# Performance work log

Hardware: AMD Instinct MI355X
Metric: run time of the kernel (lower is better)

Reference implementation:

```python
import jax, jax.numpy as jnp
import numpy as np

N = 100000      # nodes
F_IN = 500      # num_features
H = 128         # num_hidden
C = 40          # num_classes
E = 3200000     # structural edges
K = 5           # knn neighbors


def setup_inputs() -> dict:
    key = jax.random.key(0)
    ks = jax.random.split(key, 9)
    x = jax.random.normal(ks[0], (N, F_IN), dtype=jnp.float32)
    edge_index = jax.random.randint(ks[1], (2, E), 0, N, dtype=jnp.int64)
    # knn graph: source i repeated K times, targets random (stand-in for cosine-KNN)
    src = jnp.repeat(jnp.arange(N, dtype=jnp.int64), K)
    dst = jax.random.randint(ks[2], (K * N,), 0, N, dtype=jnp.int64)
    edge_index_knn = jnp.stack([src, dst])
    s = lambda f: np.float32(1.0 / np.sqrt(f))
    W1 = jax.random.normal(ks[3], (F_IN, H), jnp.float32) * s(F_IN)
    b1 = jnp.zeros((H,), jnp.float32)
    W2 = jax.random.normal(ks[4], (2 * H, C), jnp.float32) * s(2 * H)
    b2 = jnp.zeros((C,), jnp.float32)
    Wlin = jax.random.normal(ks[5], (C, 2 * C), jnp.float32) * s(2 * C)  # torch Linear layout [out,in]
    blin = jnp.zeros((C,), jnp.float32)
    return {"x": x, "edge_index": edge_index, "edge_index_knn": edge_index_knn,
            "W1": W1, "b1": b1, "W2": W2, "b2": b2, "Wlin": Wlin, "blin": blin}


def gcn_conv(x, W, b, edge_index):
    # PyG GCNConv: add self-loops, symmetric normalization deg^-1/2 A deg^-1/2, x@W, scatter-add, +bias
    n = x.shape[0]
    loop = jnp.arange(n, dtype=edge_index.dtype)
    row = jnp.concatenate([edge_index[0], loop])  # sources (gathered)
    col = jnp.concatenate([edge_index[1], loop])  # targets (scattered)
    deg = jax.ops.segment_sum(jnp.ones_like(col, x.dtype), col, num_segments=n)
    dinv = jnp.where(deg > 0, jax.lax.rsqrt(jnp.maximum(deg, 1e-12)), 0.0).astype(x.dtype)
    norm = dinv[row] * dinv[col]                      # [E+n]
    h = x @ W                                          # [n, out]
    agg = jax.ops.segment_sum(h[row] * norm[:, None], col, num_segments=n)
    return agg + b


def reference(x, edge_index, edge_index_knn, W1, b1, W2, b2, Wlin, blin):
    h1 = gcn_conv(x, W1, b1, edge_index)
    h1_2 = gcn_conv(x, W1, b1, edge_index_knn)
    R1 = jax.nn.relu(jnp.concatenate([h1, h1_2], axis=1))  # dropout identity (eval mode)
    h2 = gcn_conv(R1, W2, b2, edge_index)
    h2_2 = gcn_conv(R1, W2, b2, edge_index_knn)
    R2 = jnp.concatenate([h2, h2_2], axis=1)
    logits = R2 @ Wlin.T + blin
    return jax.nn.log_softmax(logits, axis=1)
```

## Files before the change

### kernel.cpp

```cpp
#include <hip/hip_runtime.h>
#include <stdint.h>

#define NN   100000
#define FIN  500
#define HID  128
#define KP1  512
#define K2   256
#define CO   40
#define NPQ  80
#define NBUCK 391
#define CAPB_S 9216
#define CAPB_K 1536

typedef __attribute__((ext_vector_type(8))) short short8;
typedef __attribute__((ext_vector_type(4))) float float4v;
typedef __attribute__((address_space(3))) unsigned int as3_u32;
typedef __attribute__((address_space(1))) unsigned int as1_u32;

__device__ __forceinline__ unsigned short f2bf(float f) {
  unsigned u = __float_as_uint(f);
  u = u + 0x7fffu + ((u >> 16) & 1u);
  return (unsigned short)(u >> 16);
}
__device__ __forceinline__ float bf2f(unsigned short s) {
  return __uint_as_float(((unsigned)s) << 16);
}
__device__ __forceinline__ void gl_lds16(const void* g, void* l) {
  __builtin_amdgcn_global_load_lds((const as1_u32*)g, (as3_u32*)l, 16, 0, 0);
}

__global__ __launch_bounds__(256) void k_bin(
    const int* __restrict__ ei, int nS, int nb1S, int* __restrict__ gcur_s, int* __restrict__ gbin_s,
    const int* __restrict__ eik, int nK, int* __restrict__ gcur_k, int* __restrict__ gbin_k) {
  __shared__ int cnt[NBUCK];
  __shared__ int base[NBUCK];
  const int b = blockIdx.x;
  const bool knn = (b >= nb1S);
  const int* src = knn ? eik      : ei;
  const int* tgt = knn ? eik + nK : ei + nS;
  const int n    = knn ? nK : nS;
  int* gcur      = knn ? gcur_k : gcur_s;
  int* gbin      = knn ? gbin_k : gbin_s;
  const int capb = knn ? CAPB_K : CAPB_S;
  const int ebase = (knn ? b - nb1S : b) * 4096;
  const int t = threadIdx.x;

  for (int i = t; i < NBUCK; i += 256) cnt[i] = 0;
  __syncthreads();
  int s[16], g[16];
#pragma unroll
  for (int i = 0; i < 16; ++i) {
    const int e = ebase + i * 256 + t;
    const bool v = e < n;
    s[i] = v ? src[e] : 0;
    g[i] = v ? tgt[e] : -1;
    if (v) atomicAdd(&cnt[g[i] >> 8], 1);
  }
  __syncthreads();
  for (int i = t; i < NBUCK; i += 256) {
    const int c = cnt[i];
    base[i] = c ? atomicAdd(&gcur[i], c) : 0;
    cnt[i] = 0;
  }
  __syncthreads();
#pragma unroll
  for (int i = 0; i < 16; ++i) {
    if (g[i] >= 0) {
      const int bkt = g[i] >> 8;
      const int pos = base[bkt] + atomicAdd(&cnt[bkt], 1);
      if (pos < capb) gbin[bkt * capb + pos] = (s[i] << 8) | (g[i] & 255);
    }
  }
}

__global__ __launch_bounds__(512) void k_bscan(const int* __restrict__ gcur_s, int* __restrict__ bscan_s,
                                               const int* __restrict__ gcur_k, int* __restrict__ bscan_k) {
  __shared__ int sd[512];
  const int* gcur = blockIdx.x ? gcur_k : gcur_s;
  int* bscan      = blockIdx.x ? bscan_k : bscan_s;
  const int t = threadIdx.x;
  const int v = (t < NBUCK) ? gcur[t] : 0;
  sd[t] = v;
  __syncthreads();
  for (int off = 1; off < 512; off <<= 1) {
    const int x = (t >= off) ? sd[t - off] : 0;
    __syncthreads(); sd[t] += x; __syncthreads();
  }
  if (t < NBUCK) bscan[t] = sd[t] - v;
}

__global__ __launch_bounds__(256) void k_csr(
    const int* __restrict__ gcur_s, const int* __restrict__ gbin_s, const int* __restrict__ bscan_s,
    int* __restrict__ rp_s, int2* __restrict__ colw_s, float* __restrict__ dinv_s,
    const int* __restrict__ gcur_k, const int* __restrict__ gbin_k, const int* __restrict__ bscan_k,
    int* __restrict__ rp_k, int2* __restrict__ colw_k, float* __restrict__ dinv_k) {
  __shared__ int cnt[256];
  __shared__ int base[256];
  const int b0 = blockIdx.x;
  const bool knn = (b0 >= NBUCK);
  const int b = knn ? b0 - NBUCK : b0;
  const int* gcur  = knn ? gcur_k  : gcur_s;
  const int* gbin  = knn ? gbin_k  : gbin_s;
  const int* bscan = knn ? bscan_k : bscan_s;
  int* rp     = knn ? rp_k   : rp_s;
  int2* colw  = knn ? colw_k : colw_s;
  float* dinv = knn ? dinv_k : dinv_s;
  const int capb = knn ? CAPB_K : CAPB_S;
  const int t = threadIdx.x;
  int nB = gcur[b]; if (nB > capb) nB = capb;
  const int gb0 = b * capb;
  const int gbase = bscan[b];

  cnt[t] = 0;
  __syncthreads();
  for (int i = t; i < nB; i += 256) atomicAdd(&cnt[gbin[gb0 + i] & 255], 1);
  __syncthreads();
  const int myc = cnt[t];
  base[t] = myc;
  __syncthreads();
  for (int off = 1; off < 256; off <<= 1) {
    const int x = (t >= off) ? base[t - off] : 0;
    __syncthreads(); base[t] += x; __syncthreads();
  }
  const int excl = base[t] - myc;
  const int tg = b * 256 + t;
  if (tg < NN) { rp[tg] = gbase + excl; dinv[tg] = rsqrtf((float)(myc + 1)); }
  if (tg == NN) rp[NN] = gbase + excl;
  __syncthreads();
  base[t] = excl; cnt[t] = 0;
  __syncthreads();
  for (int i = t; i < nB; i += 256) {
    const int e = gbin[gb0 + i];
    const int tl = e & 255;
    const int pos = atomicAdd(&cnt[tl], 1);
    colw[gbase + base[tl] + pos] = make_int2(e >> 8, 0);
  }
}

__global__ __launch_bounds__(256) void k_fuse(
    int2* __restrict__ colw_s, const float* __restrict__ dinv_s, int nS, int nbF,
    int2* __restrict__ colw_k, const float* __restrict__ dinv_k, int nK) {
  const int b = blockIdx.x;
  if (b < nbF) {
    const int i = b * 256 + threadIdx.x;
    if (i < nS) {
      const int s = colw_s[i].x;
      colw_s[i].y = __float_as_int(dinv_s[s]);
    }
  } else {
    const int i = (b - nbF) * 256 + threadIdx.x;
    if (i < nK) {
      const int s = colw_k[i].x;
      colw_k[i].y = __float_as_int(dinv_k[s]);
    }
  }
}

__global__ void k_w1t(const float* __restrict__ W1, unsigned short* __restrict__ W1T) {
  int idx = blockIdx.x * 256 + threadIdx.x;
  int n = idx >> 9, k = idx & 511;
  float v = (k < FIN) ? W1[k * HID + n] : 0.f;
  W1T[idx] = f2bf(v);
}
__global__ void k_wpq(const float* __restrict__ W2, const float* __restrict__ Wl,
                      const float* __restrict__ b2, const float* __restrict__ bl,
                      unsigned short* __restrict__ WpqT, float* __restrict__ cb) {
  const int idx = blockIdx.x * 256 + threadIdx.x;
  const int n = idx >> 8, k = idx & 255;
  const int o = (n < CO) ? n : n - CO;
  const int joff = (n < CO) ? 0 : CO;
  float s = 0.f;
#pragma unroll 8
  for (int j = 0; j < CO; ++j) s += W2[k * CO + j] * Wl[o * NPQ + joff + j];
  WpqT[n * K2 + k] = f2bf(s);
  if (blockIdx.x == 0 && threadIdx.x < CO) {
    const int oo = threadIdx.x;
    float c = bl[oo];
    for (int j = 0; j < CO; ++j) c += b2[j] * (Wl[oo * NPQ + j] + Wl[oo * NPQ + CO + j]);
    cb[oo] = c;
  }
}

__global__ __launch_bounds__(256) void k_gemm1(const float* __restrict__ x,
    const unsigned short* __restrict__ W1T, const float* __restrict__ zbuf,
    unsigned short* __restrict__ H1b) {
  __shared__ float Als[1024 * 4];
  __shared__ unsigned short Bls[512 * 8];
  const int t = threadIdx.x;
  const int wv = t >> 6, lane = t & 63;
  const int qd = lane >> 4, mr = lane & 15;
  const int m0 = blockIdx.x * 128;

  float4v acc[2][8];
  const float4v zf4 = {0.f, 0.f, 0.f, 0.f};
#pragma unroll
  for (int a = 0; a < 2; ++a)
#pragma unroll
    for (int b = 0; b < 8; ++b) acc[a][b] = zf4;

  for (int kk = 0; kk < 16; ++kk) {
    const int k0 = kk * 32;
    __syncthreads();
#pragma unroll
    for (int i = 0; i < 4; ++i) {
      const int cb = (wv * 4 + i) * 64;
      const int q = cb + lane;
      const int kg = q >> 7, m = q & 127;
      const int gm = m0 + m, kb = k0 + kg * 4;
      const float* gp = (gm < NN && kb < FIN) ? (x + (size_t)gm * FIN + kb) : zbuf;
      gl_lds16(gp, &Als[cb * 4]);
    }
#pragma unroll
    for (int i = 0; i < 2; ++i) {
      const int cb = (wv * 2 + i) * 64;
      const int q = cb + lane;
      const int kg = q >> 7, n = q & 127;
      const unsigned short* gp = W1T + n * KP1 + k0 + kg * 8;
      gl_lds16(gp, &Bls[cb * 8]);
    }
    __syncthreads();
    short8 af[2];
#pragma unroll
    for (int rt = 0; rt < 2; ++rt) {
      const int m = wv * 32 + rt * 16 + mr;
      const float4v a0 = *(const float4v*)&Als[((2 * qd) * 128 + m) * 4];
      const float4v a1 = *(const float4v*)&Als[((2 * qd + 1) * 128 + m) * 4];
      short8 f;
      f[0] = (short)f2bf(a0[0]); f[1] = (short)f2bf(a0[1]);
      f[2] = (short)f2bf(a0[2]); f[3] = (short)f2bf(a0[3]);
      f[4] = (short)f2bf(a1[0]); f[5] = (short)f2bf(a1[1]);
      f[6] = (short)f2bf(a1[2]); f[7] = (short)f2bf(a1[3]);
      af[rt] = f;
    }
#pragma unroll
    for (int ct = 0; ct < 8; ++ct) {
      const short8 bf = *(const short8*)&Bls[(qd * 128 + ct * 16 + mr) * 8];
      acc[0][ct] = __builtin_amdgcn_mfma_f32_16x16x32_bf16(af[0], bf, acc[0][ct], 0, 0, 0);
      acc[1][ct] = __builtin_amdgcn_mfma_f32_16x16x32_bf16(af[1], bf, acc[1][ct], 0, 0, 0);
    }
  }
#pragma unroll
  for (int rt = 0; rt < 2; ++rt) {
    const int rb = m0 + wv * 32 + rt * 16 + qd * 4;
#pragma unroll
    for (int ct = 0; ct < 8; ++ct) {
      const int col = ct * 16 + mr;
#pragma unroll
      for (int j = 0; j < 4; ++j) {
        const int r = rb + j;
        if (r < NN) H1b[(size_t)r * HID + col] = f2bf(acc[rt][ct][j]);
      }
    }
  }
}

__global__ __launch_bounds__(256) void k_gemm2(const unsigned short* __restrict__ R1b,
    const unsigned short* __restrict__ WpqT, const unsigned short* __restrict__ zbuf,
    unsigned short* __restrict__ PQ) {
  __shared__ unsigned short Als[512 * 8];
  __shared__ unsigned short Bls[320 * 8];
  const int t = threadIdx.x;
  const int wv = t >> 6, lane = t & 63;
  const int qd = lane >> 4, mr = lane & 15;
  const int m0 = blockIdx.x * 128;

  float4v acc[2][5];
  const float4v zf4 = {0.f, 0.f, 0.f, 0.f};
#pragma unroll
  for (int a = 0; a < 2; ++a)
#pragma unroll
    for (int b = 0; b < 5; ++b) acc[a][b] = zf4;

  for (int kk = 0; kk < 8; ++kk) {
    const int k0 = kk * 32;
    __syncthreads();
#pragma unroll
    for (int i = 0; i < 2; ++i) {
      const int cb = (wv * 2 + i) * 64;
      const int q = cb + lane;
      const int kg = q >> 7, m = q & 127;
      const int gm = m0 + m;
      const unsigned short* gp = (gm < NN) ? (R1b + (size_t)gm * K2 + k0 + kg * 8) : zbuf;
      gl_lds16(gp, &Als[cb * 8]);
    }
    {
      const int cb = wv * 64;
      const int q = cb + lane;
      const int kg = q / 80, n = q % 80;
      gl_lds16(WpqT + n * K2 + k0 + kg * 8, &Bls[cb * 8]);
      if (wv == 0) {
        const int cb2 = 4 * 64;
        const int q2 = cb2 + lane;
        const int kg2 = q2 / 80, n2 = q2 % 80;
        gl_lds16(WpqT + n2 * K2 + k0 + kg2 * 8, &Bls[cb2 * 8]);
      }
    }
    __syncthreads();
    short8 af[2];
#pragma unroll
    for (int rt = 0; rt < 2; ++rt)
      af[rt] = *(const short8*)&Als[(qd * 128 + wv * 32 + rt * 16 + mr) * 8];
#pragma unroll
    for (int ct = 0; ct < 5; ++ct) {
      const short8 bf = *(const short8*)&Bls[(qd * 80 + ct * 16 + mr) * 8];
      acc[0][ct] = __builtin_amdgcn_mfma_f32_16x16x32_bf16(af[0], bf, acc[0][ct], 0, 0, 0);
      acc[1][ct] = __builtin_amdgcn_mfma_f32_16x16x32_bf16(af[1], bf, acc[1][ct], 0, 0, 0);
    }
  }
#pragma unroll
  for (int rt = 0; rt < 2; ++rt) {
    const int rb = m0 + wv * 32 + rt * 16 + qd * 4;
#pragma unroll
    for (int ct = 0; ct < 5; ++ct) {
      const int col = ct * 16 + mr;
#pragma unroll
      for (int j = 0; j < 4; ++j) {
        const int r = rb + j;
        if (r < NN) PQ[(size_t)r * NPQ + col] = f2bf(acc[rt][ct][j]);
      }
    }
  }
}

__device__ __forceinline__ void ld8(const int2* __restrict__ cw, int base, int e1, bool full,
                                    int2* __restrict__ q) {
  if (full) {
#pragma unroll
    for (int j = 0; j < 8; ++j) q[j] = cw[base + j];
  } else {
    const int e1c = e1 - 1;
#pragma unroll
    for (int j = 0; j < 8; ++j) {
      const int ee = base + j;
      int2 t = cw[(ee < e1) ? ee : e1c];
      t.y = (ee < e1) ? t.y : 0;
      q[j] = t;
    }
  }
}
__device__ __forceinline__ void g8(const int2* __restrict__ q,
    const unsigned* __restrict__ H32, int lane, unsigned* __restrict__ d) {
#pragma unroll
  for (int j = 0; j < 8; ++j) d[j] = H32[(size_t)q[j].x * 64 + lane];
}
__device__ __forceinline__ void f8(const int2* __restrict__ q, const unsigned* __restrict__ d,
                                   float& ax, float& ay) {
#pragma unroll
  for (int j = 0; j < 8; ++j) {
    const float w = __int_as_float(q[j].y);
    ax += w * __uint_as_float(d[j] << 16);
    ay += w * __uint_as_float(d[j] & 0xffff0000u);
  }
}

__global__ __launch_bounds__(256) void k_agg1(
    const int* __restrict__ rp_s, const int2* __restrict__ colw_s, const float* __restrict__ dinv_s,
    const int* __restrict__ rp_k, const int2* __restrict__ colw_k, const float* __restrict__ dinv_k,
    const unsigned short* __restrict__ H, const float* __restrict__ bias,
    unsigned short* __restrict__ out) {
  const int wv = threadIdx.x >> 6, lane = threadIdx.x & 63;
  const int c = blockIdx.x * 4 + wv;
  if (c >= NN) return;
  const unsigned* H32 = (const unsigned*)H;
  const int e0s = __builtin_amdgcn_readfirstlane(rp_s[c]);
  const int e1s = __builtin_amdgcn_readfirstlane(rp_s[c + 1]);
  const int e0k = __builtin_amdgcn_readfirstlane(rp_k[c]);
  const int e1k = __builtin_amdgcn_readfirstlane(rp_k[c + 1]);
  const int nbS = (e1s - e0s + 7) >> 3;
  const int nbK = (e1k - e0k + 7) >> 3;

  int2 q0[8], q1[8], qk[8];
  unsigned d0[8], d1[8], dk[8];
  const unsigned pc = H32[(size_t)c * 64 + lane];
  if (nbS > 0) { ld8(colw_s, e0s, e1s, e0s + 8 <= e1s, q0); g8(q0, H32, lane, d0); }
  if (nbS > 1) { ld8(colw_s, e0s + 8, e1s, e0s + 16 <= e1s, q1); g8(q1, H32, lane, d1); }
  if (nbK > 0) { ld8(colw_k, e0k, e1k, e0k + 8 <= e1k, qk); g8(qk, H32, lane, dk); }

  const float dcs = dinv_s[c], dck = dinv_k[c];
  const float slo = __uint_as_float(pc << 16);
  const float shi = __uint_as_float(pc & 0xffff0000u);
  float ax = dcs * slo, ay = dcs * shi;
  float bx = dck * slo, by = dck * shi;

  int b = 0;
  while (b + 2 < nbS) {
    f8(q0, d0, ax, ay);
    {
      const int bs = e0s + (b + 2) * 8;
      ld8(colw_s, bs, e1s, bs + 8 <= e1s, q0);
      g8(q0, H32, lane, d0);
    }
    f8(q1, d1, ax, ay);
    if (b + 3 < nbS) {
      const int bs = e0s + (b + 3) * 8;
      ld8(colw_s, bs, e1s, bs + 8 <= e1s, q1);
      g8(q1, H32, lane, d1);
    }
    b += 2;
  }
  if (b < nbS) f8(q0, d0, ax, ay);
  if (b + 1 < nbS) f8(q1, d1, ax, ay);

  if (nbK > 0) f8(qk, dk, bx, by);
  for (int bk = 1; bk < nbK; ++bk) {
    const int bs = e0k + bk * 8;
    ld8(colw_k, bs, e1k, bs + 8 <= e1k, qk);
    g8(qk, H32, lane, dk);
    f8(qk, dk, bx, by);
  }

  const float2 bb = ((const float2*)bias)[lane];
  const float o0 = fmaxf(dcs * ax + bb.x, 0.f);
  const float o1 = fmaxf(dcs * ay + bb.y, 0.f);
  const float o2 = fmaxf(dck * bx + bb.x, 0.f);
  const float o3 = fmaxf(dck * by + bb.y, 0.f);
  unsigned* orow = (unsigned*)(out + (size_t)c * K2);
  orow[lane]      = (unsigned)f2bf(o0) | ((unsigned)f2bf(o1) << 16);
  orow[64 + lane] = (unsigned)f2bf(o2) | ((unsigned)f2bf(o3) << 16);
}

__global__ __launch_bounds__(256) void k_aggf(
    const int* __restrict__ rp_s, const int2* __restrict__ colw_s, const float* __restrict__ dinv_s,
    const int* __restrict__ rp_k, const int2* __restrict__ colw_k, const float* __restrict__ dinv_k,
    const unsigned short* __restrict__ PQ, const float* __restrict__ cb,
    float* __restrict__ out) {
  const int wv = threadIdx.x >> 6, lane = threadIdx.x & 63;
  const int c = blockIdx.x * 4 + wv;
  if (c >= NN) return;
  const unsigned* PQ32 = (const unsigned*)PQ;
  const int g = lane / 20;
  const int l = lane % 20;
  float sx = 0.f, sy = 0.f, kx = 0.f, ky = 0.f;
  if (g < 3) {
    {
      const int e1 = rp_s[c + 1];
      int e = rp_s[c] + g;
      for (; e + 9 < e1; e += 12) {
        const int2 q0 = colw_s[e], q1 = colw_s[e + 3], q2 = colw_s[e + 6], q3 = colw_s[e + 9];
        const unsigned d0 = PQ32[(size_t)q0.x * 40 + l];
        const unsigned d1 = PQ32[(size_t)q1.x * 40 + l];
        const unsigned d2 = PQ32[(size_t)q2.x * 40 + l];
        const unsigned d3 = PQ32[(size_t)q3.x * 40 + l];
        const float w0 = __int_as_float(q0.y), w1 = __int_as_float(q1.y);
        const float w2 = __int_as_float(q2.y), w3 = __int_as_float(q3.y);
        sx += w0 * __uint_as_float(d0 << 16) + w1 * __uint_as_float(d1 << 16)
            + w2 * __uint_as_float(d2 << 16) + w3 * __uint_as_float(d3 << 16);
        sy += w0 * __uint_as_float(d0 & 0xffff0000u) + w1 * __uint_as_float(d1 & 0xffff0000u)
            + w2 * __uint_as_float(d2 & 0xffff0000u) + w3 * __uint_as_float(d3 & 0xffff0000u);
      }
      for (; e < e1; e += 3) {
        const int2 q = colw_s[e];
        const unsigned d = PQ32[(size_t)q.x * 40 + l];
        const float w = __int_as_float(q.y);
        sx += w * __uint_as_float(d << 16);
        sy += w * __uint_as_float(d & 0xffff0000u);
      }
    }
    {
      const int e1 = rp_k[c + 1];
      int e = rp_k[c] + g;
      for (; e < e1; e += 3) {
        const int2 q = colw_k[e];
        const unsigned d = PQ32[(size_t)q.x * 40 + 20 + l];
        const float w = __int_as_float(q.y);
        kx += w * __uint_as_float(d << 16);
        ky += w * __uint_as_float(d & 0xffff0000u);
      }
    }
  }
  sx += __shfl(sx, lane + 20) + __shfl(sx, lane + 40);
  sy += __shfl(sy, lane + 20) + __shfl(sy, lane + 40);
  kx += __shfl(kx, lane + 20) + __shfl(kx, lane + 40);
  ky += __shfl(ky, lane + 20) + __shfl(ky, lane + 40);

  float lo = 0.f, hi = 0.f;
  if (lane < 20) {
    const float dcs = dinv_s[c], dck = dinv_k[c];
    const unsigned dP = PQ32[(size_t)c * 40 + lane];
    const unsigned dQ = PQ32[(size_t)c * 40 + 20 + lane];
    const float2 cbb = ((const float2*)cb)[lane];
    lo = dcs * (sx + dcs * __uint_as_float(dP << 16))
       + dck * (kx + dck * __uint_as_float(dQ << 16)) + cbb.x;
    hi = dcs * (sy + dcs * __uint_as_float(dP & 0xffff0000u))
       + dck * (ky + dck * __uint_as_float(dQ & 0xffff0000u)) + cbb.y;
  }
  float m = (lane < 20) ? fmaxf(lo, hi) : -3.4e38f;
#pragma unroll
  for (int off = 1; off < 64; off <<= 1) m = fmaxf(m, __shfl_xor(m, off));
  float s = (lane < 20) ? (expf(lo - m) + expf(hi - m)) : 0.f;
#pragma unroll
  for (int off = 1; off < 64; off <<= 1) s += __shfl_xor(s, off);
  const float lse = m + logf(s);
  if (lane < 20) {
    float2 o; o.x = lo - lse; o.y = hi - lse;
    ((float2*)(out + (size_t)c * CO))[lane] = o;
  }
}

extern "C" void kernel_launch(void* const* d_in, const int* in_sizes, int n_in,
                              void* d_out, int out_size, void* d_ws, size_t ws_size,
                              hipStream_t stream) {
  const float* x  = (const float*)d_in[0];
  const int* ei   = (const int*)d_in[1];
  const int* eik  = (const int*)d_in[2];
  const float* W1 = (const float*)d_in[3];
  const float* b1 = (const float*)d_in[4];
  const float* W2 = (const float*)d_in[5];
  const float* b2 = (const float*)d_in[6];
  const float* Wl = (const float*)d_in[7];
  const float* bl = (const float*)d_in[8];
  float* out = (float*)d_out;
  const int E  = in_sizes[1] / 2;
  const int EK = in_sizes[2] / 2;

  char* p = (char*)d_ws;
  size_t off = 0;
  auto alloc = [&](size_t bytes) -> void* {
    void* r = (void*)(p + off);
    off += (bytes + 255) & ~(size_t)255;
    return r;
  };
  int* gcur_s = (int*)alloc((size_t)NBUCK * 4);
  int* gcur_k = (int*)alloc((size_t)NBUCK * 4);
  void* zbuf = alloc(256);
  const size_t zero_span = off;
  int* bscan_s = (int*)alloc((size_t)NBUCK * 4);
  int* bscan_k = (int*)alloc((size_t)NBUCK * 4);
  float* dinv_s = (float*)alloc((size_t)NN * 4);
  float* dinv_k = (float*)alloc((size_t)NN * 4);
  int* rp_s = (int*)alloc((size_t)(NN + 1) * 4);
  int* rp_k = (int*)alloc((size_t)(NN + 1) * 4);
  unsigned short* W1T = (unsigned short*)alloc((size_t)HID * KP1 * 2);
  unsigned short* WpqT = (unsigned short*)alloc((size_t)NPQ * K2 * 2);
  float* cbv = (float*)alloc((size_t)CO * 4);
  int* gbin_s = (int*)alloc((size_t)NBUCK * CAPB_S * 4);
  int* gbin_k = (int*)alloc((size_t)NBUCK * CAPB_K * 4);
  int2* colw_s = (int2*)alloc((size_t)E * 8);
  int2* colw_k = (int2*)alloc((size_t)EK * 8);
  unsigned short* H1b = (unsigned short*)alloc((size_t)NN * HID * 2);
  unsigned short* R1b = (unsigned short*)alloc((size_t)NN * K2 * 2);
  unsigned short* PQ = H1b;

  hipMemsetAsync(d_ws, 0, zero_span, stream);

  const int nb1S = (E + 4095) / 4096;
  const int nb1K = (EK + 4095) / 4096;
  k_bin<<<nb1S + nb1K, 256, 0, stream>>>(ei, E, nb1S, gcur_s, gbin_s, eik, EK, gcur_k, gbin_k);
  k_bscan<<<2, 512, 0, stream>>>(gcur_s, bscan_s, gcur_k, bscan_k);
  k_csr<<<2 * NBUCK, 256, 0, stream>>>(gcur_s, gbin_s, bscan_s, rp_s, colw_s, dinv_s,
                                       gcur_k, gbin_k, bscan_k, rp_k, colw_k, dinv_k);
  const int nbF = (E + 255) / 256;
  const int nbFk = (EK + 255) / 256;
  k_fuse<<<nbF + nbFk, 256, 0, stream>>>(colw_s, dinv_s, E, nbF, colw_k, dinv_k, EK);

  k_w1t<<<(HID * KP1) / 256, 256, 0, stream>>>(W1, W1T);
  k_wpq<<<NPQ, 256, 0, stream>>>(W2, Wl, b2, bl, WpqT, cbv);

  k_gemm1<<<(NN + 127) / 128, 256, 0, stream>>>(x, W1T, (const float*)zbuf, H1b);
  const int nbAgg = (NN + 3) / 4;
  k_agg1<<<nbAgg, 256, 0, stream>>>(rp_s, colw_s, dinv_s, rp_k, colw_k, dinv_k, H1b, b1, R1b);

  k_gemm2<<<(NN + 127) / 128, 256, 0, stream>>>(R1b, WpqT, (const unsigned short*)zbuf, PQ);
  k_aggf<<<nbAgg, 256, 0, stream>>>(rp_s, colw_s, dinv_s, rp_k, colw_k, dinv_k, PQ, cbv, out);
}
```

Measured before the change: 722.8 us.

## Double-buffer GEMM1 LDS tiles and halve the row tile to 64

GEMM1 now uses two LDS buffers and prefetches the next K-slice with direct global-to-LDS loads while the current slice goes through the MFMAs, synchronized with explicit vmcnt waits and raw barriers. The M tile per block drops from 128 to 64 rows, so each wave computes one 16-row tile and the grid doubles. The aim is to hide the global load latency of the fp32 x matrix and raise occupancy. In exchange, each W1T tile is loaded twice as often per row, and the hand-written vmcnt(4) count must match the number of loads issued per stage to stay correct.

Measured after the change: 714.2 us. No clear change (-1.2%).

```diff
diff --git a/kernel.cpp b/kernel.cpp
--- a/kernel.cpp
+++ b/kernel.cpp
@@ -184,72 +184,75 @@
 __global__ __launch_bounds__(256) void k_gemm1(const float* __restrict__ x,
     const unsigned short* __restrict__ W1T, const float* __restrict__ zbuf,
     unsigned short* __restrict__ H1b) {
-  __shared__ float Als[1024 * 4];
-  __shared__ unsigned short Bls[512 * 8];
+  __shared__ float Als[2][512 * 4];
+  __shared__ unsigned short Bls[2][512 * 8];
   const int t = threadIdx.x;
   const int wv = t >> 6, lane = t & 63;
   const int qd = lane >> 4, mr = lane & 15;
-  const int m0 = blockIdx.x * 128;
-
-  float4v acc[2][8];
+  const int m0 = blockIdx.x * 64;
+
+  float4v acc[8];
   const float4v zf4 = {0.f, 0.f, 0.f, 0.f};
 #pragma unroll
-  for (int a = 0; a < 2; ++a)
-#pragma unroll
-    for (int b = 0; b < 8; ++b) acc[a][b] = zf4;
-
-  for (int kk = 0; kk < 16; ++kk) {
+  for (int b = 0; b < 8; ++b) acc[b] = zf4;
+
+  auto stage = [&](int kk, int pb) {
     const int k0 = kk * 32;
-    __syncthreads();
-#pragma unroll
-    for (int i = 0; i < 4; ++i) {
-      const int cb = (wv * 4 + i) * 64;
+#pragma unroll
+    for (int i = 0; i < 2; ++i) {
+      const int cb = i * 256 + wv * 64;
       const int q = cb + lane;
-      const int kg = q >> 7, m = q & 127;
+      const int kg = q >> 6, m = q & 63;
       const int gm = m0 + m, kb = k0 + kg * 4;
       const float* gp = (gm < NN && kb < FIN) ? (x + (size_t)gm * FIN + kb) : zbuf;
-      gl_lds16(gp, &Als[cb * 4]);
+      gl_lds16(gp, &Als[pb][cb * 4]);
     }
 #pragma unroll
     for (int i = 0; i < 2; ++i) {
-      const int cb = (wv * 2 + i) * 64;
+      const int cb = i * 256 + wv * 64;
       const int q = cb + lane;
       const int kg = q >> 7, n = q & 127;
-      const unsigned short* gp = W1T + n * KP1 + k0 + kg * 8;
-      gl_lds16(gp, &Bls[cb * 8]);
-    }
-    __syncthreads();
-    short8 af[2];
-#pragma unroll
-    for (int rt = 0; rt < 2; ++rt) {
-      const int m = wv * 32 + rt * 16 + mr;
-      const float4v a0 = *(const float4v*)&Als[((2 * qd) * 128 + m) * 4];
-      const float4v a1 = *(const float4v*)&Als[((2 * qd + 1) * 128 + m) * 4];
-      short8 f;
-      f[0] = (short)f2bf(a0[0]); f[1] = (short)f2bf(a0[1]);
-      f[2] = (short)f2bf(a0[2]); f[3] = (short)f2bf(a0[3]);
-      f[4] = (short)f2bf(a1[0]); f[5] = (short)f2bf(a1[1]);
-      f[6] = (short)f2bf(a1[2]); f[7] = (short)f2bf(a1[3]);
-      af[rt] = f;
+      gl_lds16(W1T + n * KP1 + k0 + kg * 8, &Bls[pb][cb * 8]);
+    }
+  };
+
+  stage(0, 0);
+  for (int kk = 0; kk < 16; ++kk) {
+    const int cur = kk & 1;
+    if (kk + 1 < 16) {
+      stage(kk + 1, cur ^ 1);
+      asm volatile("s_waitcnt vmcnt(4)" ::: "memory");
+    } else {
+      asm volatile("s_waitcnt vmcnt(0)" ::: "memory");
+    }
+    __builtin_amdgcn_s_barrier();
+
+    short8 af;
+    {
+      const int m = wv * 16 + mr;
+      const float4v a0 = *(const float4v*)&Als[cur][((2 * qd) * 64 + m) * 4];
+      const float4v a1 = *(const float4v*)&Als[cur][((2 * qd + 1) * 64 + m) * 4];
+      af[0] = (short)f2bf(a0[0]); af[1] = (short)f2bf(a0[1]);
+      af[2] = (short)f2bf(a0[2]); af[3] = (short)f2bf(a0[3]);
+      af[4] = (short)f2bf(a1[0]); af[5] = (short)f2bf(a1[1]);
+      af[6] = (short)f2bf(a1[2]); af[7] = (short)f2bf(a1[3]);
     }
 #pragma unroll
     for (int ct = 0; ct < 8; ++ct) {
-      const short8 bf = *(const short8*)&Bls[(qd * 128 + ct * 16 + mr) * 8];
-      acc[0][ct] = __builtin_amdgcn_mfma_f32_16x16x32_bf16(af[0], bf, acc[0][ct], 0, 0, 0);
-      acc[1][ct] = __builtin_amdgcn_mfma_f32_16x16x32_bf16(af[1], bf, acc[1][ct], 0, 0, 0);
-    }
-  }
-#pragma unroll
-  for (int rt = 0; rt < 2; ++rt) {
-    const int rb = m0 + wv * 32 + rt * 16 + qd * 4;
-#pragma unroll
-    for (int ct = 0; ct < 8; ++ct) {
-      const int col = ct * 16 + mr;
-#pragma unroll
-      for (int j = 0; j < 4; ++j) {
-        const int r = rb + j;
-        if (r < NN) H1b[(size_t)r * HID + col] = f2bf(acc[rt][ct][j]);
-      }
+      const short8 bf = *(const short8*)&Bls[cur][(qd * 128 + ct * 16 + mr) * 8];
+      acc[ct] = __builtin_amdgcn_mfma_f32_16x16x32_bf16(af, bf, acc[ct], 0, 0, 0);
+    }
+    __builtin_amdgcn_s_barrier();
+  }
+
+  const int rb = m0 + wv * 16 + qd * 4;
+#pragma unroll
+  for (int ct = 0; ct < 8; ++ct) {
+    const int col = ct * 16 + mr;
+#pragma unroll
+    for (int j = 0; j < 4; ++j) {
+      const int r = rb + j;
+      if (r < NN) H1b[(size_t)r * HID + col] = f2bf(acc[ct][j]);
     }
   }
 }
@@ -556,7 +559,7 @@
   k_w1t<<<(HID * KP1) / 256, 256, 0, stream>>>(W1, W1T);
   k_wpq<<<NPQ, 256, 0, stream>>>(W2, Wl, b2, bl, WpqT, cbv);
 
-  k_gemm1<<<(NN + 127) / 128, 256, 0, stream>>>(x, W1T, (const float*)zbuf, H1b);
+  k_gemm1<<<(NN + 63) / 64, 256, 0, stream>>>(x, W1T, (const float*)zbuf, H1b);
   const int nbAgg = (NN + 3) / 4;
   k_agg1<<<nbAgg, 256, 0, stream>>>(rp_s, colw_s, dinv_s, rp_k, colw_k, dinv_k, H1b, b1, R1b);
 
```
